# Performance work log

Hardware: AMD Instinct MI355X
Metric: run time of the kernel (lower is better)

Reference implementation:

```python
import jax, jax.numpy as jnp
import numpy as np

B, S, H = 32, 512, 768
NH, HD = 8, 96
NC = 3
SEP = 102
NEG = -1e9


def telu(x):
    return x * jnp.tanh(jnp.exp(x))


def setup_inputs() -> dict:
    rng = np.random.default_rng(0)
    key = jax.random.key(0)
    ks = jax.random.split(key, 16)
    # ragged premise/hypothesis spans: [CLS] premise [SEP] hypothesis [SEP] pad
    s1 = rng.integers(64, 256, size=B)
    s2 = rng.integers(s1 + 32, 500)
    ids = rng.integers(1000, 30000, size=(B, S))  # avoid accidental SEP ids
    for i in range(B):
        ids[i, 0] = 101
        ids[i, s1[i]] = SEP
        ids[i, s2[i]] = SEP
        ids[i, s2[i] + 1:] = 0
    pos = np.arange(S)[None, :]
    am = (pos <= s2[:, None]).astype(np.int32)

    def lin(k, i, o):
        return jax.random.normal(k, (i, o), jnp.float32) * 0.02

    return dict(
        hidden_states=jax.random.normal(ks[0], (B, S, H), jnp.float32),
        input_ids=jnp.asarray(ids, jnp.int32),
        attention_mask=jnp.asarray(am, jnp.int32),
        fe_w1=lin(ks[1], H, 512), fe_b1=jnp.zeros(512), fe_g=jnp.ones(512), fe_be=jnp.zeros(512),
        fe_w2=lin(ks[2], 512, 128), fe_b2=jnp.zeros(128),
        al_w1=lin(ks[3], 2 * H, 768), al_b1=jnp.zeros(768),
        al_w2=lin(ks[4], 768, 128), al_b2=jnp.zeros(128),
        mha_wq=lin(ks[5], H, H), mha_bq=jnp.zeros(H),
        mha_wk=lin(ks[6], H, H), mha_bk=jnp.zeros(H),
        mha_wv=lin(ks[7], H, H), mha_bv=jnp.zeros(H),
        mha_wo=lin(ks[8], H, H), mha_bo=jnp.zeros(H),
        dp_w=lin(ks[9], H, 128), dp_b=jnp.zeros(128),
        ap_w=lin(ks[10], H, 128), ap_b=jnp.zeros(128),
        cl_w1=lin(ks[11], 512, 64), cl_b1=jnp.zeros(64),
        cl_w2=lin(ks[12], 64, NC), cl_b2=jnp.zeros(NC),
    )


def reference(hidden_states, input_ids, attention_mask,
              fe_w1, fe_b1, fe_g, fe_be, fe_w2, fe_b2,
              al_w1, al_b1, al_w2, al_b2,
              mha_wq, mha_bq, mha_wk, mha_bk, mha_wv, mha_bv, mha_wo, mha_bo,
              dp_w, dp_b, ap_w, ap_b, cl_w1, cl_b1, cl_w2, cl_b2):
    hs = hidden_states
    am = attention_mask.astype(hs.dtype)
    sep = (input_ids == SEP)
    pos = jnp.arange(S)[None, :]
    s1 = jnp.argmax(sep, axis=1)            # first SEP
    s2 = (S - 1) - jnp.argmax(sep[:, ::-1], axis=1)  # second SEP
    prem = ((pos >= 1) & (pos < s1[:, None])).astype(hs.dtype)   # premise span [1, s1)
    hyp = ((pos > s1[:, None]) & (pos < s2[:, None])).astype(hs.dtype)  # hypothesis (s1, s2)

    def mmean(x, m):  # masked mean over seq: x [B,S,H], m [B,S]
        return jnp.einsum('bsh,bs->bh', x, m) / jnp.clip(m.sum(1, keepdims=True), 1e-9, None)

    # pooled + mean + max representations -> feature_extractor
    pooled = hs[:, 0]
    mean_rep = mmean(hs, am)
    max_rep = jnp.max(jnp.where(am[..., None] > 0, hs, NEG), axis=1)
    h = (pooled + mean_rep + max_rep) @ fe_w1 + fe_b1
    h = (h - h.mean(-1, keepdims=True)) / jnp.sqrt(h.var(-1, keepdims=True) + 1e-5) * fe_g + fe_be
    feat = telu(h @ fe_w2 + fe_b2)

    # sentence diff head
    sent_diff = jnp.abs(mmean(hs, prem) - mmean(hs, hyp))
    diff_rep = telu(sent_diff @ dp_w + dp_b)

    # cross attention: hypothesis queries attend to premise keys/values
    q = (hs @ mha_wq + mha_bq).reshape(B, S, NH, HD)
    k = (hs @ mha_wk + mha_bk).reshape(B, S, NH, HD)
    v = (hs @ mha_wv + mha_bv).reshape(B, S, NH, HD)
    scores = jnp.einsum('bqhd,bkhd->bhqk', q, k) / np.sqrt(HD).astype(np.float32)
    scores = jnp.where(prem[:, None, None, :] > 0, scores, NEG)
    attn = jax.nn.softmax(scores, axis=-1)
    ctx = jnp.einsum('bhqk,bkhd->bqhd', attn, v).reshape(B, S, H) @ mha_wo + mha_bo
    attn_rep = telu(mmean(ctx, hyp) @ ap_w + ap_b)

    # word alignment (both directions share one similarity matrix)
    sim = jnp.einsum('bsd,btd->bst', hs, hs)
    w_p2h = jax.nn.softmax(jnp.where(hyp[:, None, :] > 0, sim, NEG), axis=-1)
    al1 = mmean(jnp.einsum('bst,btd->bsd', w_p2h, hs), prem)
    w_h2p = jax.nn.softmax(jnp.where(prem[:, None, :] > 0, sim, NEG), axis=-1)
    al2 = mmean(jnp.einsum('bst,btd->bsd', w_h2p, hs), hyp)
    align_rep = telu((jnp.concatenate([al1, al2], -1) @ al_w1 + al_b1) @ al_w2 + al_b2)

    combined = jnp.concatenate([feat, diff_rep, attn_rep, align_rep], -1)  # [B, 512]
    logits = telu(combined @ cl_w1 + cl_b1) @ cl_w2 + cl_b2
    return logits
```

## Files before the change

kernel.cpp:

```cpp
#include <hip/hip_runtime.h>
#include <hip/hip_bf16.h>
#include <math.h>

#define SS 512
#define HH 768
#define NEGV -1e9f
#define APAD 100

typedef float f32x4 __attribute__((ext_vector_type(4)));
typedef __bf16 bf16x8 __attribute__((ext_vector_type(8)));

__device__ __forceinline__ float telu_f(float x){ return x * tanhf(expf(x)); }

__device__ __forceinline__ short f2bf(float x){
  __hip_bfloat16 h = __float2bfloat16(x);
  return __builtin_bit_cast(short, h);
}
__device__ __forceinline__ float b2f(short s){
  __hip_bfloat16 h = __builtin_bit_cast(__hip_bfloat16, s);
  return __bfloat162float(h);
}

__device__ __forceinline__ void gl_lds16(const void* g, void* l){
  __builtin_amdgcn_global_load_lds((const __attribute__((address_space(1))) void*)g,
                                   (__attribute__((address_space(3))) void*)l, 16, 0, 0);
}

__device__ __forceinline__ float wred_max(float v){
  #pragma unroll
  for (int o=32;o>0;o>>=1) v = fmaxf(v, __shfl_xor(v, o));
  return v;
}
__device__ __forceinline__ float wred_sum(float v){
  #pragma unroll
  for (int o=32;o>0;o>>=1) v += __shfl_xor(v, o);
  return v;
}

__global__ __launch_bounds__(512) void k_scan(const int* __restrict__ ids, const int* __restrict__ am,
                       int* s1a, int* s2a, float* invnam, float* invnp, float* invnh,
                       float* __restrict__ uacc, float* __restrict__ v1g, float* __restrict__ v2g){
  int b = blockIdx.x, tid = threadIdx.x;
  __shared__ int mn, mx, cnt;
  if (tid==0){ mn = 1<<30; mx = -1; cnt = 0; }
  __syncthreads();
  int id = ids[b*SS+tid];
  if (id==102){ atomicMin(&mn, tid); atomicMax(&mx, tid); }
  atomicAdd(&cnt, am[b*SS+tid]);
  #pragma unroll
  for (int i=0;i<4;i++) uacc[(size_t)b*2048 + tid + i*512] = 0.f;
  v1g[b*SS+tid] = 0.f;
  v2g[b*SS+tid] = 0.f;
  __syncthreads();
  if (tid==0){
    int s1 = mn; if (s1 > 255) s1 = 255; if (s1 < 1) s1 = 1;
    int s2 = mx; if (s2 < s1+1) s2 = s1+1; if (s2 > 511) s2 = 511;
    s1a[b]=s1; s2a[b]=s2;
    invnam[b] = 1.f/fmaxf((float)cnt, 1e-9f);
    invnp[b]  = 1.f/fmaxf((float)(s1-1), 1e-9f);
    invnh[b]  = 1.f/fmaxf((float)(s2-s1-1), 1e-9f);
  }
}

__global__ __launch_bounds__(256) void k_g2(const float* __restrict__ hs, const int* __restrict__ amask,
    const int* __restrict__ s1a, const int* __restrict__ s2a,
    short* __restrict__ hsb, short* __restrict__ hsl, float4* __restrict__ repp,
    const float* __restrict__ wq, const float* __restrict__ wk, const float* __restrict__ wv,
    short* __restrict__ Wt){
  __shared__ __align__(16) char smem[16896];
  int id = blockIdx.x, tid = threadIdx.x;
  if (id < 768){
    int b = id&31, hc = (id>>5)%6, sc = id/192;
    int* ams = (int*)smem;
    float4* rb4 = (float4*)(smem + 512);
    int sbase = sc*128;
    if (tid < 128) ams[tid] = amask[b*SS + sbase + tid];
    __syncthreads();
    int s1 = s1a[b], s2 = s2a[b];
    int hlane = tid & 31, srow = tid >> 5;
    int h0 = hc*128 + hlane*4;
    float sm[4]={0,0,0,0}, sp[4]={0,0,0,0}, sh[4]={0,0,0,0};
    float mxv[4]={NEGV,NEGV,NEGV,NEGV};
    for (int si = srow; si < 128; si += 8){
      int s = sbase + si;
      float4 x = *(const float4*)(hs + ((size_t)(b*SS+s))*HH + h0);
      float xv[4] = {x.x,x.y,x.z,x.w};
      bool am = ams[si] > 0;
      bool ip = (s>=1 && s<s1), ih = (s>s1 && s<s2);
      short hi4[4], lo4[4];
      #pragma unroll
      for (int c=0;c<4;c++){
        if (am){ sm[c]+=xv[c]; mxv[c]=fmaxf(mxv[c],xv[c]); }
        if (ip) sp[c]+=xv[c];
        if (ih) sh[c]+=xv[c];
        hi4[c] = f2bf(xv[c]);
        lo4[c] = f2bf(xv[c] - b2f(hi4[c]));
      }
      *(short4*)(hsb + ((size_t)(b*SS+s))*HH + h0) = *(short4*)hi4;
      *(short4*)(hsl + ((size_t)(b*SS+s))*HH + h0) = *(short4*)lo4;
    }
    #pragma unroll
    for (int c=0;c<4;c++) rb4[srow*128 + hlane*4+c] = make_float4(sm[c], mxv[c], sp[c], sh[c]);
    __syncthreads();
    if (tid < 128){
      float4 a = rb4[tid];
      #pragma unroll
      for (int r=1;r<8;r++){
        float4 v = rb4[r*128 + tid];
        a.x += v.x; a.y = fmaxf(a.y, v.y); a.z += v.z; a.w += v.w;
      }
      repp[(((size_t)(b*6+hc))*4 + sc)*128 + tid] = a;
    }
  } else {
    int w = id - 768;
    int k0 = (w%24)*32, n0 = ((w/24)%24)*32, which = w/576;
    const float* W = which==0? wq : (which==1? wk : wv);
    float (*tl)[33] = (float(*)[33])smem;
    int r = tid>>3, c4 = (tid&7)*4;
    float4 v = *(const float4*)(W + (size_t)(k0+r)*HH + n0 + c4);
    tl[r][c4+0]=v.x; tl[r][c4+1]=v.y; tl[r][c4+2]=v.z; tl[r][c4+3]=v.w;
    __syncthreads();
    short4 o;
    o.x = f2bf(tl[c4+0][r]); o.y = f2bf(tl[c4+1][r]);
    o.z = f2bf(tl[c4+2][r]); o.w = f2bf(tl[c4+3][r]);
    *(short4*)(Wt + (size_t)which*HH*HH + (size_t)(n0+r)*HH + k0 + c4) = o;
  }
}

__device__ __forceinline__ void build_vec(const float4* __restrict__ repp, const float* __restrict__ hs,
    const float* __restrict__ invnam, const float* __restrict__ invnp, const float* __restrict__ invnh,
    int b, int tid, bool want_sdiff, float* xs){
  for (int h = tid; h < HH; h += 256){
    int hc = h>>7, hr = h&127;
    float S=0.f, M=NEGV, P=0.f, Hh=0.f;
    #pragma unroll
    for (int sc=0; sc<4; sc++){
      float4 v = repp[(((size_t)(b*6+hc))*4 + sc)*128 + hr];
      S += v.x; M = fmaxf(M, v.y); P += v.z; Hh += v.w;
    }
    if (want_sdiff) xs[h] = fabsf(P*invnp[b] - Hh*invnh[b]);
    else            xs[h] = hs[((size_t)(b*SS))*HH + h] + S*invnam[b] + M;
  }
}

__global__ __launch_bounds__(256) void k_smallA(const float4* __restrict__ repp, const float* __restrict__ hs,
    const float* __restrict__ invnam, const float* __restrict__ invnp, const float* __restrict__ invnh,
    const float* __restrict__ fe_w1, const float* __restrict__ fe_b1, float* __restrict__ featd,
    const float* __restrict__ dpw, const float* __restrict__ dpb, float* __restrict__ comb){
  __shared__ float xs[HH];
  __shared__ float psum[2][128];
  int id = blockIdx.x, tid = threadIdx.x;
  int jj = tid & 127, half = tid >> 7;
  if (id < 128){
    int b = id&31, j0 = (id>>5)*128;
    build_vec(repp, hs, invnam, invnp, invnh, b, tid, false, xs);
    __syncthreads();
    float a = 0.f;
    #pragma unroll 8
    for (int i = half*384; i < half*384+384; i++)
      a += xs[i]*fe_w1[(size_t)i*512 + j0 + jj];
    psum[half][jj] = a;
    __syncthreads();
    if (tid < 128)
      featd[(size_t)b*512 + j0 + tid] = fe_b1[j0+tid] + psum[0][tid] + psum[1][tid];
  } else {
    int b = id - 128;
    build_vec(repp, hs, invnam, invnp, invnh, b, tid, true, xs);
    __syncthreads();
    float a = 0.f;
    #pragma unroll 8
    for (int i = half*384; i < half*384+384; i++)
      a += xs[i]*dpw[(size_t)i*128 + jj];
    psum[half][jj] = a;
    __syncthreads();
    if (tid < 128)
      comb[b*512 + 128 + tid] = telu_f(dpb[tid] + psum[0][tid] + psum[1][tid]);
  }
}

__global__ __launch_bounds__(256) void k_mm(const short* __restrict__ hsb, const short* __restrict__ hsl,
    const short* __restrict__ Wt,
    const float* __restrict__ bq, const float* __restrict__ bk, const float* __restrict__ bv,
    short* __restrict__ qbh, short* __restrict__ kbh, float* __restrict__ vb,
    const int* __restrict__ s1a, const int* __restrict__ s2a, float* __restrict__ sim){
  __shared__ __align__(16) char smem[32768];
  int id = blockIdx.x;
  int tid = threadIdx.x, lane = tid&63, wave = tid>>6;
  int wm = wave>>1, wn = wave&1;
  int lm = lane&15, lq = lane>>4;
  if (id < 1536){
    int which, local;
    if (id < 768){ which=0; local=id; }
    else if (id < 1152){ which=1; local=id-768; }
    else { which=2; local=id-1152; }
    int r8 = local & 7, n = (local>>3)%6, gq = local/48;
    int rt = gq*8 + r8;
    int n0 = n*128;
    int r0, b;
    if (which==0){ r0 = rt*128; b = r0>>9; }
    else { b = rt>>1; r0 = b*512 + (rt&1)*128; }
    int s1 = s1a[b], s2 = s2a[b];
    int s0 = r0 & (SS-1);
    if (which==0){ if (s0 >= s2 || s0 + 127 <= s1) return; }
    else { if (s0 >= s1) return; }
    const float* bias = which==0? bq : (which==1? bk : bv);
    const short* Wb = Wt + (size_t)which*HH*HH;
    short* As = (short*)smem;
    short* Bs = As + 4096;
    f32x4 acc[4][4];
    #pragma unroll
    for (int i=0;i<4;i++)
      #pragma unroll
      for (int j=0;j<4;j++) acc[i][j] = (f32x4){0.f,0.f,0.f,0.f};
    for (int k0=0;k0<HH;k0+=32){
      __syncthreads();
      #pragma unroll
      for (int t=0;t<2;t++){
        int c = tid + t*256;
        int ib = c>>6, l = c&63;
        int row = ib*16 + (l&15);
        int kk  = k0 + (l>>4)*8;
        gl_lds16(hsb + (size_t)(r0+row)*HH + kk, As + c*8);
        gl_lds16(Wb  + (size_t)(n0+row)*HH + kk, Bs + c*8);
      }
      __syncthreads();
      bf16x8 af[4], bfv[4];
      #pragma unroll
      for (int i=0;i<4;i++) af[i]  = *(const bf16x8*)&As[((wm*4+i)*64 + lane)*8];
      #pragma unroll
      for (int j=0;j<4;j++) bfv[j] = *(const bf16x8*)&Bs[((wn*4+j)*64 + lane)*8];
      #pragma unroll
      for (int i=0;i<4;i++)
        #pragma unroll
        for (int j=0;j<4;j++)
          acc[i][j] = __builtin_amdgcn_mfma_f32_16x16x32_bf16(af[i], bfv[j], acc[i][j], 0, 0, 0);
    }
    #pragma unroll
    for (int i=0;i<4;i++){
      #pragma unroll
      for (int j=0;j<4;j++){
        int col = n0 + wn*64 + j*16 + lm;
        float bcol = bias[col];
        #pragma unroll
        for (int r4=0;r4<4;r4++){
          int row = r0 + wm*64 + i*16 + lq*4 + r4;
          int s = row & (SS-1);
          float val = acc[i][j][r4] + bcol;
          if (which==0){
            if (s > s1 && s < s2) qbh[(size_t)row*HH + col] = f2bf(val);
          } else if (s >= 1 && s < s1){
            size_t o = ((size_t)(b*256+s))*HH + col;
            if (which==1) kbh[o] = f2bf(val); else vb[o] = val;
          }
        }
      }
    }
  } else {
    int local = id - 1536;
    int b = (local&7) + 8*(local>>7);
    int t = (local>>3)&15;
    int s0 = (t>>2)*128, t0 = (t&3)*128;
    int s2 = s2a[b];
    if (s0 >= s2 || t0 >= s2) return;
    short* Ah = (short*)smem;
    short* Al = Ah + 4096;
    short* Bh = Ah + 8192;
    short* Bl = Ah + 12288;
    const size_t base = (size_t)b*SS*HH;
    f32x4 acc[4][4];
    #pragma unroll
    for (int i=0;i<4;i++)
      #pragma unroll
      for (int j=0;j<4;j++) acc[i][j] = (f32x4){0.f,0.f,0.f,0.f};
    for (int k0=0;k0<HH;k0+=32){
      __syncthreads();
      #pragma unroll
      for (int t2=0;t2<2;t2++){
        int c = tid + t2*256;
        int ib = c>>6, l = c&63;
        int row = ib*16 + (l&15);
        int kk  = k0 + (l>>4)*8;
        gl_lds16(hsb + base + (size_t)(s0+row)*HH + kk, Ah + c*8);
        gl_lds16(hsl + base + (size_t)(s0+row)*HH + kk, Al + c*8);
        gl_lds16(hsb + base + (size_t)(t0+row)*HH + kk, Bh + c*8);
        gl_lds16(hsl + base + (size_t)(t0+row)*HH + kk, Bl + c*8);
      }
      __syncthreads();
      bf16x8 ah[4], al[4], bh[4], bl[4];
      #pragma unroll
      for (int i=0;i<4;i++){
        ah[i] = *(const bf16x8*)&Ah[((wm*4+i)*64 + lane)*8];
        al[i] = *(const bf16x8*)&Al[((wm*4+i)*64 + lane)*8];
      }
      #pragma unroll
      for (int j=0;j<4;j++){
        bh[j] = *(const bf16x8*)&Bh[((wn*4+j)*64 + lane)*8];
        bl[j] = *(const bf16x8*)&Bl[((wn*4+j)*64 + lane)*8];
      }
      #pragma unroll
      for (int i=0;i<4;i++)
        #pragma unroll
        for (int j=0;j<4;j++){
          acc[i][j] = __builtin_amdgcn_mfma_f32_16x16x32_bf16(ah[i], bh[j], acc[i][j], 0, 0, 0);
          acc[i][j] = __builtin_amdgcn_mfma_f32_16x16x32_bf16(ah[i], bl[j], acc[i][j], 0, 0, 0);
          acc[i][j] = __builtin_amdgcn_mfma_f32_16x16x32_bf16(al[i], bh[j], acc[i][j], 0, 0, 0);
        }
    }
    #pragma unroll
    for (int i=0;i<4;i++){
      #pragma unroll
      for (int j=0;j<4;j++){
        int col = t0 + wn*64 + j*16 + lm;
        #pragma unroll
        for (int r4=0;r4<4;r4++){
          int row = s0 + wm*64 + i*16 + lq*4 + r4;
          sim[((size_t)(b*SS+row))*SS + col] = acc[i][j][r4];
        }
      }
    }
  }
}

__global__ __launch_bounds__(256) void k_attn_simsm(const short* __restrict__ qbh, const short* __restrict__ kbh,
    const int* __restrict__ s1a, const int* __restrict__ s2a, float* __restrict__ uacc,
    const float* __restrict__ sim, float* __restrict__ v1g, float* __restrict__ v2g){
  __shared__ __align__(16) char smem[64000];
  int id = blockIdx.x, tid = threadIdx.x;
  int wave = tid>>6, lane = tid&63;
  if (id < 2048){
    int b = id&31, h = (id>>5)&7, zc = id>>8;
    int s1 = s1a[b], s2 = s2a[b];
    int qs = s1 + 1 + zc*64;
    if (qs >= s2) return;
    short* Ks = (short*)smem;
    short* Qs = Ks + 256*APAD;
    int lm = lane&15, lq = lane>>4;
    int jmax = (s1+15)>>4;
    int krows = jmax<<4;
    for (int i = tid; i < krows*12; i += 256){
      int r = i/12, c = i - r*12;
      *(int4*)&Ks[r*APAD + c*8] = *(const int4*)(kbh + ((size_t)(b*256+r))*HH + h*96 + c*8);
    }
    for (int i = tid; i < 64*12; i += 256){
      int r = i/12, c = i - r*12;
      int q = qs + r;
      int4 v = {0,0,0,0};
      if (q < SS) v = *(const int4*)(qbh + ((size_t)(b*SS+q))*HH + h*96 + c*8);
      *(int4*)&Qs[r*APAD + c*8] = v;
    }
    __syncthreads();
    f32x4 acc[16];
    #pragma unroll
    for (int j=0;j<16;j++) acc[j] = (f32x4){0.f,0.f,0.f,0.f};
    #pragma unroll
    for (int ks=0; ks<3; ks++){
      bf16x8 a = *(const bf16x8*)&Qs[(wave*16+lm)*APAD + ks*32 + lq*8];
      #pragma unroll
      for (int j=0;j<16;j++){
        if (j < jmax){
          bf16x8 bfr = *(const bf16x8*)&Ks[(j*16+lm)*APAD + ks*32 + lq*8];
          acc[j] = __builtin_amdgcn_mfma_f32_16x16x32_bf16(a, bfr, acc[j], 0, 0, 0);
        }
      }
    }
    const float scale = 0.1020620726f;
    float uj[16];
    #pragma unroll
    for (int j=0;j<16;j++) uj[j]=0.f;
    int qrow_base = qs + wave*16 + lq*4;
    #pragma unroll
    for (int r=0;r<4;r++){
      float m = -1e30f;
      float sc[16];
      #pragma unroll
      for (int j=0;j<16;j++){
        int c = j*16 + lm;
        float s = (c>=1 && c<s1) ? acc[j][r]*scale : -1e30f;
        sc[j] = s; m = fmaxf(m, s);
      }
      #pragma unroll
      for (int o=1;o<16;o<<=1) m = fmaxf(m, __shfl_xor(m, o));
      float ssum = 0.f;
      #pragma unroll
      for (int j=0;j<16;j++){ float p = expf(sc[j]-m); sc[j]=p; ssum += p; }
      #pragma unroll
      for (int o=1;o<16;o<<=1) ssum += __shfl_xor(ssum, o);
      bool rvalid = (qrow_base + r) < s2;
      float inv = rvalid ? 1.f/ssum : 0.f;
      #pragma unroll
      for (int j=0;j<16;j++) uj[j] += sc[j]*inv;
    }
    #pragma unroll
    for (int j=0;j<16;j++){
      if (j < jmax){
        float v = uj[j];
        v += __shfl_xor(v, 16);
        v += __shfl_xor(v, 32);
        if (lq==0 && v != 0.f)
          atomicAdd(&uacc[((size_t)(b*8+h))*256 + j*16 + lm], v);
      }
    }
  } else {
    int l = id - 2048;
    int b = l&31, cy = l>>5;
    int s1 = s1a[b], s2 = s2a[b];
    int r0 = cy*64;
    float* av = (float*)smem;
    for (int i=tid;i<2*4*SS;i+=256) av[i]=0.f;
    __syncthreads();
    for (int r = r0 + wave; r < r0+64; r += 4){
      int t0,t1,which;
      if (r>=1 && r<s1){ t0=s1+1; t1=s2; which=0; }
      else if (r>s1 && r<s2){ t0=1; t1=s1; which=1; }
      else continue;
      const float* row = sim + ((size_t)(b*SS+r))*SS;
      float vals[7]; float mx=-1e30f;
      #pragma unroll
      for (int j=0;j<7;j++){
        int t = t0 + lane + 64*j;
        vals[j] = (t<t1) ? row[t] : -1e30f;
        mx = fmaxf(mx, vals[j]);
      }
      mx = wred_max(mx);
      float ssum=0.f;
      #pragma unroll
      for (int j=0;j<7;j++){
        int t = t0+lane+64*j;
        vals[j] = (t<t1)? expf(vals[j]-mx) : 0.f;
        ssum += vals[j];
      }
      ssum = wred_sum(ssum);
      float inv = 1.f/ssum;
      #pragma unroll
      for (int j=0;j<7;j++){
        int t = t0+lane+64*j;
        if (t<t1) av[(which*4 + wave)*SS + t] += vals[j]*inv;
      }
    }
    __syncthreads();
    for (int t=tid;t<SS;t+=256){
      float a0 = av[0*SS+t]+av[1*SS+t]+av[2*SS+t]+av[3*SS+t];
      float a1 = av[4*SS+t]+av[5*SS+t]+av[6*SS+t]+av[7*SS+t];
      if (a0 != 0.f) atomicAdd(&v1g[b*SS+t], a0);
      if (a1 != 0.f) atomicAdd(&v2g[b*SS+t], a1);
    }
  }
}

__global__ __launch_bounds__(256) void k_ctx_alvec(const float* __restrict__ uacc, const float* __restrict__ vb,
    const int* __restrict__ s1a, const float* __restrict__ invnh, float* __restrict__ cmg,
    const float* __restrict__ hs, const float* __restrict__ v1g, const float* __restrict__ v2g,
    const float* __restrict__ invnp, float* __restrict__ catg){
  __shared__ __align__(16) char smem[9216];
  int id = blockIdx.x, tid = threadIdx.x;
  if (id < 192){
    int b = id&31, i0 = (id>>5)*128;
    int s1 = s1a[b]; int nk = s1-1;
    float inh = invnh[b];
    float* us = (float*)smem;
    float* ps = us + 2048;
    for (int idx=tid; idx<2048; idx+=256) us[idx] = uacc[(size_t)b*2048 + idx];
    __syncthreads();
    int ii = tid & 127, half = tid >> 7;
    int i = i0 + ii;
    int h = i/96;
    float a = 0.f;
    int lo = 1 + half*128;
    int hi = nk < (lo+127) ? nk : (lo+127);
    for (int sl=lo; sl<=hi; sl++)
      a += us[h*256+sl]*vb[((size_t)(b*256+sl))*HH + i];
    ps[half*128 + ii] = a;
    __syncthreads();
    if (tid < 128)
      cmg[(size_t)b*HH + i0 + tid] = (ps[tid] + ps[128+tid])*inh;
  } else {
    int l = id - 192;
    int b = l&31, d0 = (l>>5)*64;
    float* sv1 = (float*)smem;
    float* sv2 = sv1 + 512;
    float* p1  = sv2 + 512;
    float* p2  = p1 + 256;
    for (int t=tid;t<SS;t+=256){ sv1[t]=v1g[b*SS+t]; sv2[t]=v2g[b*SS+t]; }
    __syncthreads();
    int d = d0 + (tid&63), ch = tid>>6;
    float a1=0.f, a2=0.f;
    for (int t=ch*128; t<ch*128+128; t++){
      float x = hs[((size_t)(b*SS+t))*HH + d];
      a1 += sv1[t]*x; a2 += sv2[t]*x;
    }
    p1[ch*64 + (tid&63)]=a1; p2[ch*64 + (tid&63)]=a2;
    __syncthreads();
    if (tid < 64){
      float s1_ = p1[tid]+p1[64+tid]+p1[128+tid]+p1[192+tid];
      float s2_ = p2[tid]+p2[64+tid]+p2[128+tid]+p2[192+tid];
      catg[(size_t)b*1536 + d0 + tid]       = s1_*invnp[b];
      catg[(size_t)b*1536 + 768 + d0 + tid] = s2_*invnh[b];
    }
  }
}

template<int K>
__device__ __forceinline__ void gemv_ct(const float* __restrict__ x, const float* __restrict__ W,
    const float* __restrict__ bias, float* __restrict__ y, int b, int j0, int tid,
    float* xs, float* psum){
  for (int i=tid;i<K;i+=256) xs[i] = x[(size_t)b*K + i];
  __syncthreads();
  int jj = tid & 127, half = tid >> 7;
  int j = j0 + jj;
  float a = 0.f;
  #pragma unroll 8
  for (int i = half*(K/2); i < (half+1)*(K/2); i++)
    a += xs[i]*W[(size_t)i*HH + j];
  psum[half*128 + jj] = a;
  __syncthreads();
  if (tid < 128)
    y[(size_t)b*HH + j0 + tid] = bias[j0+tid] + psum[tid] + psum[128+tid];
}

__global__ __launch_bounds__(256) void k_gemvB(const float* __restrict__ cmg, const float* __restrict__ wo,
    const float* __restrict__ bo, float* __restrict__ accg,
    const float* __restrict__ catg, const float* __restrict__ al_w1, const float* __restrict__ al_b1,
    float* __restrict__ tmpg){
  __shared__ float xs[1536];
  __shared__ float psum[256];
  int id = blockIdx.x, tid = threadIdx.x;
  if (id < 192){
    gemv_ct<768>(cmg, wo, bo, accg, id&31, (id>>5)*128, tid, xs, psum);
  } else {
    int l = id-192;
    gemv_ct<1536>(catg, al_w1, al_b1, tmpg, l&31, (l>>5)*128, tid, xs, psum);
  }
}

__global__ __launch_bounds__(256) void k_tailsC(const float* __restrict__ accg, const float* __restrict__ apw,
    const float* __restrict__ apb, const float* __restrict__ tmpg, const float* __restrict__ al_w2,
    const float* __restrict__ al_b2, float* __restrict__ comb,
    const float* __restrict__ featd, const float* __restrict__ g, const float* __restrict__ be,
    const float* __restrict__ w2, const float* __restrict__ b2){
  __shared__ __align__(16) float smem[1664];
  int id = blockIdx.x, tid = threadIdx.x;
  if (id < 64){
    float* xs = smem;
    float* psum = smem + HH;
    const float *x, *W, *bias; int b, off;
    if (id < 32){ b = id; x=accg; W=apw; bias=apb; off=256; }
    else { b = id-32; x=tmpg; W=al_w2; bias=al_b2; off=384; }
    for (int i=tid;i<HH;i+=256) xs[i] = x[(size_t)b*HH + i];
    __syncthreads();
    int jj = tid & 127, half = tid >> 7;
    float a = 0.f;
    #pragma unroll 8
    for (int i = half*384; i < half*384+384; i++)
      a += xs[i]*W[(size_t)i*128 + jj];
    psum[half*128 + jj] = a;
    __syncthreads();
    if (tid < 128)
      comb[b*512 + off + tid] = telu_f(bias[tid] + psum[tid] + psum[128+tid]);
  } else {
    int b = id - 64;
    float* hv  = smem;
    float* hn  = hv + 512;
    float* red = hn + 512;
    float* ps  = red + 256;
    hv[tid] = featd[(size_t)b*512 + tid];
    hv[tid+256] = featd[(size_t)b*512 + tid + 256];
    __syncthreads();
    red[tid] = hv[tid] + hv[tid+256];
    __syncthreads();
    for (int st=128; st>0; st>>=1){ if (tid<st) red[tid]+=red[tid+st]; __syncthreads(); }
    float mean = red[0]*(1.f/512.f);
    __syncthreads();
    float d0 = hv[tid]-mean, d1 = hv[tid+256]-mean;
    red[tid] = d0*d0 + d1*d1;
    __syncthreads();
    for (int st=128; st>0; st>>=1){ if (tid<st) red[tid]+=red[tid+st]; __syncthreads(); }
    float inv = 1.f/sqrtf(red[0]*(1.f/512.f) + 1e-5f);
    __syncthreads();
    hn[tid]     = d0*inv*g[tid]     + be[tid];
    hn[tid+256] = d1*inv*g[tid+256] + be[tid+256];
    __syncthreads();
    int jj = tid & 127, half = tid >> 7;
    float a = 0.f;
    #pragma unroll 8
    for (int k = half*256; k < half*256+256; k++)
      a += hn[k]*w2[k*128 + jj];
    ps[half*128 + jj] = a;
    __syncthreads();
    if (tid < 128)
      comb[b*512 + tid] = telu_f(b2[tid] + ps[tid] + ps[128+tid]);
  }
}

__global__ __launch_bounds__(64) void k_cls(const float* __restrict__ comb,
    const float* __restrict__ w1, const float* __restrict__ b1,
    const float* __restrict__ w2, const float* __restrict__ b2, float* __restrict__ out){
  int b=blockIdx.x, tid=threadIdx.x;
  __shared__ float cb[512];
  __shared__ float t1[64];
  for (int i=tid;i<512;i+=64) cb[i]=comb[b*512+i];
  __syncthreads();
  float a = b1[tid];
  for (int k=0;k<512;k++) a += cb[k]*w1[(size_t)k*64+tid];
  t1[tid]=telu_f(a);
  __syncthreads();
  if (tid<3){
    float o = b2[tid];
    for (int k=0;k<64;k++) o += t1[k]*w2[k*3+tid];
    out[b*3+tid]=o;
  }
}

extern "C" void kernel_launch(void* const* d_in, const int* in_sizes, int n_in,
                              void* d_out, int out_size, void* d_ws, size_t ws_size,
                              hipStream_t stream){
  const float* hs   = (const float*)d_in[0];
  const int*   ids  = (const int*)d_in[1];
  const int*   amask= (const int*)d_in[2];
  const float* fe_w1= (const float*)d_in[3];
  const float* fe_b1= (const float*)d_in[4];
  const float* fe_g = (const float*)d_in[5];
  const float* fe_be= (const float*)d_in[6];
  const float* fe_w2= (const float*)d_in[7];
  const float* fe_b2= (const float*)d_in[8];
  const float* al_w1= (const float*)d_in[9];
  const float* al_b1= (const float*)d_in[10];
  const float* al_w2= (const float*)d_in[11];
  const float* al_b2= (const float*)d_in[12];
  const float* wq   = (const float*)d_in[13];
  const float* bq   = (const float*)d_in[14];
  const float* wk   = (const float*)d_in[15];
  const float* bk   = (const float*)d_in[16];
  const float* wv   = (const float*)d_in[17];
  const float* bv   = (const float*)d_in[18];
  const float* wo   = (const float*)d_in[19];
  const float* bo   = (const float*)d_in[20];
  const float* dpw  = (const float*)d_in[21];
  const float* dpb  = (const float*)d_in[22];
  const float* apw  = (const float*)d_in[23];
  const float* apb  = (const float*)d_in[24];
  const float* clw1 = (const float*)d_in[25];
  const float* clb1 = (const float*)d_in[26];
  const float* clw2 = (const float*)d_in[27];
  const float* clb2 = (const float*)d_in[28];
  float* out = (float*)d_out;

  char* base = (char*)d_ws;
  size_t off = 0;
  auto alloc = [&](size_t bytes)->char*{ char* p = base + off; off += (bytes + 255) & ~(size_t)255; return p; };
  short* hsb  = (short*)alloc((size_t)32*SS*HH*2);
  short* hsl  = (short*)alloc((size_t)32*SS*HH*2);
  short* Wt   = (short*)alloc((size_t)3*HH*HH*2);
  short* qbh  = (short*)alloc((size_t)32*SS*HH*2);
  short* kbh  = (short*)alloc((size_t)32*256*HH*2);
  float* vb   = (float*)alloc((size_t)32*256*HH*4);
  float* simb = (float*)alloc((size_t)32*SS*SS*4);
  float* uacc = (float*)alloc((size_t)32*8*256*4);
  float* v1g  = (float*)alloc((size_t)32*SS*4);
  float* v2g  = (float*)alloc((size_t)32*SS*4);
  int*   s1a  = (int*)alloc(32*4);
  int*   s2a  = (int*)alloc(32*4);
  float* invnam=(float*)alloc(32*4);
  float* invnp =(float*)alloc(32*4);
  float* invnh =(float*)alloc(32*4);
  float* comb = (float*)alloc((size_t)32*512*4);
  float4* repp= (float4*)alloc((size_t)32*6*4*128*16);
  float* featd= (float*)alloc((size_t)32*512*4);
  float* catg = (float*)alloc((size_t)32*1536*4);
  float* tmpg = (float*)alloc((size_t)32*HH*4);
  float* cmg  = (float*)alloc((size_t)32*HH*4);
  float* accg = (float*)alloc((size_t)32*HH*4);

  k_scan<<<dim3(32), dim3(512), 0, stream>>>(ids, amask, s1a, s2a, invnam, invnp, invnh, uacc, v1g, v2g);
  k_g2<<<dim3(2496), dim3(256), 0, stream>>>(hs, amask, s1a, s2a, hsb, hsl, repp, wq, wk, wv, Wt);
  k_mm<<<dim3(2048), dim3(256), 0, stream>>>(hsb, hsl, Wt, bq, bk, bv, qbh, kbh, vb, s1a, s2a, simb);
  k_smallA<<<dim3(160), dim3(256), 0, stream>>>(repp, hs, invnam, invnp, invnh, fe_w1, fe_b1, featd, dpw, dpb, comb);
  k_attn_simsm<<<dim3(2304), dim3(256), 0, stream>>>(qbh, kbh, s1a, s2a, uacc, simb, v1g, v2g);
  k_ctx_alvec<<<dim3(576), dim3(256), 0, stream>>>(uacc, vb, s1a, invnh, cmg, hs, v1g, v2g, invnp, catg);
  k_gemvB<<<dim3(384), dim3(256), 0, stream>>>(cmg, wo, bo, accg, catg, al_w1, al_b1, tmpg);
  k_tailsC<<<dim3(96), dim3(256), 0, stream>>>(accg, apw, apb, tmpg, al_w2, al_b2, comb,
                                               featd, fe_g, fe_be, fe_w2, fe_b2);
  k_cls<<<dim3(32), dim3(64), 0, stream>>>(comb, clw1, clb1, clw2, clb2, out);
}
```

Measured before the change: 544.4 us.

## Double-buffer LDS in k_mm GEMMs, reorder sim blocks first, fold k_smallA in

The QKV projection and similarity GEMM tiles now double-buffer their LDS staging, so the global-to-LDS loads for the next k-slice are issued while MFMAs run on the current one. The heavier similarity blocks are moved to the start of the grid so they are scheduled early. The small gemv kernel k_smallA is merged into k_mm as extra trailing blocks, removing one launch and letting that work overlap with the GEMM tail. LDS per block grows to 64KB, which may reduce occupancy.

```diff
diff --git a/kernel.cpp b/kernel.cpp
--- a/kernel.cpp
+++ b/kernel.cpp
@@ -143,56 +143,99 @@
   }
 }
 
-__global__ __launch_bounds__(256) void k_smallA(const float4* __restrict__ repp, const float* __restrict__ hs,
-    const float* __restrict__ invnam, const float* __restrict__ invnp, const float* __restrict__ invnh,
-    const float* __restrict__ fe_w1, const float* __restrict__ fe_b1, float* __restrict__ featd,
-    const float* __restrict__ dpw, const float* __restrict__ dpb, float* __restrict__ comb){
-  __shared__ float xs[HH];
-  __shared__ float psum[2][128];
-  int id = blockIdx.x, tid = threadIdx.x;
-  int jj = tid & 127, half = tid >> 7;
-  if (id < 128){
-    int b = id&31, j0 = (id>>5)*128;
-    build_vec(repp, hs, invnam, invnp, invnh, b, tid, false, xs);
-    __syncthreads();
-    float a = 0.f;
-    #pragma unroll 8
-    for (int i = half*384; i < half*384+384; i++)
-      a += xs[i]*fe_w1[(size_t)i*512 + j0 + jj];
-    psum[half][jj] = a;
-    __syncthreads();
-    if (tid < 128)
-      featd[(size_t)b*512 + j0 + tid] = fe_b1[j0+tid] + psum[0][tid] + psum[1][tid];
-  } else {
-    int b = id - 128;
-    build_vec(repp, hs, invnam, invnp, invnh, b, tid, true, xs);
-    __syncthreads();
-    float a = 0.f;
-    #pragma unroll 8
-    for (int i = half*384; i < half*384+384; i++)
-      a += xs[i]*dpw[(size_t)i*128 + jj];
-    psum[half][jj] = a;
-    __syncthreads();
-    if (tid < 128)
-      comb[b*512 + 128 + tid] = telu_f(dpb[tid] + psum[0][tid] + psum[1][tid]);
-  }
-}
-
 __global__ __launch_bounds__(256) void k_mm(const short* __restrict__ hsb, const short* __restrict__ hsl,
     const short* __restrict__ Wt,
     const float* __restrict__ bq, const float* __restrict__ bk, const float* __restrict__ bv,
     short* __restrict__ qbh, short* __restrict__ kbh, float* __restrict__ vb,
-    const int* __restrict__ s1a, const int* __restrict__ s2a, float* __restrict__ sim){
-  __shared__ __align__(16) char smem[32768];
+    const int* __restrict__ s1a, const int* __restrict__ s2a, float* __restrict__ sim,
+    const float4* __restrict__ repp, const float* __restrict__ hs,
+    const float* __restrict__ invnam, const float* __restrict__ invnp, const float* __restrict__ invnh,
+    const float* __restrict__ fe_w1, const float* __restrict__ fe_b1, float* __restrict__ featd,
+    const float* __restrict__ dpw, const float* __restrict__ dpb, float* __restrict__ comb){
+  __shared__ __align__(16) short smem_s[32768];
   int id = blockIdx.x;
   int tid = threadIdx.x, lane = tid&63, wave = tid>>6;
   int wm = wave>>1, wn = wave&1;
   int lm = lane&15, lq = lane>>4;
-  if (id < 1536){
+  if (id < 512){
+    int local = id;
+    int b = (local&7) + 8*(local>>7);
+    int t = (local>>3)&15;
+    int s0 = (t>>2)*128, t0 = (t&3)*128;
+    int s2 = s2a[b];
+    if (s0 >= s2 || t0 >= s2) return;
+    const size_t base = (size_t)b*SS*HH;
+    auto stage = [&](int k0, int bufi){
+      short* Ah = smem_s + bufi*16384;
+      short* Al = Ah + 4096;
+      short* Bh = Ah + 8192;
+      short* Bl = Ah + 12288;
+      #pragma unroll
+      for (int t2=0;t2<2;t2++){
+        int c = tid + t2*256;
+        int ib = c>>6, l = c&63;
+        int row = ib*16 + (l&15);
+        int kk  = k0 + (l>>4)*8;
+        gl_lds16(hsb + base + (size_t)(s0+row)*HH + kk, Ah + c*8);
+        gl_lds16(hsl + base + (size_t)(s0+row)*HH + kk, Al + c*8);
+        gl_lds16(hsb + base + (size_t)(t0+row)*HH + kk, Bh + c*8);
+        gl_lds16(hsl + base + (size_t)(t0+row)*HH + kk, Bl + c*8);
+      }
+    };
+    f32x4 acc[4][4];
+    #pragma unroll
+    for (int i=0;i<4;i++)
+      #pragma unroll
+      for (int j=0;j<4;j++) acc[i][j] = (f32x4){0.f,0.f,0.f,0.f};
+    stage(0, 0);
+    __syncthreads();
+    int bufi = 0;
+    for (int k0=0;k0<HH;k0+=32){
+      if (k0+32 < HH) stage(k0+32, bufi^1);
+      short* Ah = smem_s + bufi*16384;
+      short* Al = Ah + 4096;
+      short* Bh = Ah + 8192;
+      short* Bl = Ah + 12288;
+      bf16x8 ah[4], al[4], bh[4], bl[4];
+      #pragma unroll
+      for (int i=0;i<4;i++){
+        ah[i] = *(const bf16x8*)&Ah[((wm*4+i)*64 + lane)*8];
+        al[i] = *(const bf16x8*)&Al[((wm*4+i)*64 + lane)*8];
+      }
+      #pragma unroll
+      for (int j=0;j<4;j++){
+        bh[j] = *(const bf16x8*)&Bh[((wn*4+j)*64 + lane)*8];
+        bl[j] = *(const bf16x8*)&Bl[((wn*4+j)*64 + lane)*8];
+      }
+      #pragma unroll
+      for (int i=0;i<4;i++)
+        #pragma unroll
+        for (int j=0;j<4;j++){
+          acc[i][j] = __builtin_amdgcn_mfma_f32_16x16x32_bf16(ah[i], bh[j], acc[i][j], 0, 0, 0);
+          acc[i][j] = __builtin_amdgcn_mfma_f32_16x16x32_bf16(ah[i], bl[j], acc[i][j], 0, 0, 0);
+          acc[i][j] = __builtin_amdgcn_mfma_f32_16x16x32_bf16(al[i], bh[j], acc[i][j], 0, 0, 0);
+        }
+      __syncthreads();
+      bufi ^= 1;
+    }
+    #pragma unroll
+    for (int i=0;i<4;i++){
+      #pragma unroll
+      for (int j=0;j<4;j++){
+        int col = t0 + wn*64 + j*16 + lm;
+        #pragma unroll
+        for (int r4=0;r4<4;r4++){
+          int row = s0 + wm*64 + i*16 + lq*4 + r4;
+          sim[((size_t)(b*SS+row))*SS + col] = acc[i][j][r4];
+        }
+      }
+    }
+  } else if (id < 2048){
     int which, local;
-    if (id < 768){ which=0; local=id; }
-    else if (id < 1152){ which=1; local=id-768; }
-    else { which=2; local=id-1152; }
+    int qid = id - 512;
+    if (qid < 768){ which=0; local=qid; }
+    else if (qid < 1152){ which=1; local=qid-768; }
+    else { which=2; local=qid-1152; }
     int r8 = local & 7, n = (local>>3)%6, gq = local/48;
     int rt = gq*8 + r8;
     int n0 = n*128;
@@ -205,25 +248,31 @@
     else { if (s0 >= s1) return; }
     const float* bias = which==0? bq : (which==1? bk : bv);
     const short* Wb = Wt + (size_t)which*HH*HH;
-    short* As = (short*)smem;
-    short* Bs = As + 4096;
-    f32x4 acc[4][4];
-    #pragma unroll
-    for (int i=0;i<4;i++)
-      #pragma unroll
-      for (int j=0;j<4;j++) acc[i][j] = (f32x4){0.f,0.f,0.f,0.f};
-    for (int k0=0;k0<HH;k0+=32){
-      __syncthreads();
-      #pragma unroll
-      for (int t=0;t<2;t++){
-        int c = tid + t*256;
+    auto stageq = [&](int k0, int bufi){
+      short* As = smem_s + bufi*8192;
+      short* Bs = As + 4096;
+      #pragma unroll
+      for (int t2=0;t2<2;t2++){
+        int c = tid + t2*256;
         int ib = c>>6, l = c&63;
         int row = ib*16 + (l&15);
         int kk  = k0 + (l>>4)*8;
         gl_lds16(hsb + (size_t)(r0+row)*HH + kk, As + c*8);
         gl_lds16(Wb  + (size_t)(n0+row)*HH + kk, Bs + c*8);
       }
-      __syncthreads();
+    };
+    f32x4 acc[4][4];
+    #pragma unroll
+    for (int i=0;i<4;i++)
+      #pragma unroll
+      for (int j=0;j<4;j++) acc[i][j] = (f32x4){0.f,0.f,0.f,0.f};
+    stageq(0, 0);
+    __syncthreads();
+    int bufi = 0;
+    for (int k0=0;k0<HH;k0+=32){
+      if (k0+32 < HH) stageq(k0+32, bufi^1);
+      short* As = smem_s + bufi*8192;
+      short* Bs = As + 4096;
       bf16x8 af[4], bfv[4];
       #pragma unroll
       for (int i=0;i<4;i++) af[i]  = *(const bf16x8*)&As[((wm*4+i)*64 + lane)*8];
@@ -234,6 +283,8 @@
         #pragma unroll
         for (int j=0;j<4;j++)
           acc[i][j] = __builtin_amdgcn_mfma_f32_16x16x32_bf16(af[i], bfv[j], acc[i][j], 0, 0, 0);
+      __syncthreads();
+      bufi ^= 1;
     }
     #pragma unroll
     for (int i=0;i<4;i++){
@@ -256,67 +307,34 @@
       }
     }
   } else {
-    int local = id - 1536;
-    int b = (local&7) + 8*(local>>7);
-    int t = (local>>3)&15;
-    int s0 = (t>>2)*128, t0 = (t&3)*128;
-    int s2 = s2a[b];
-    if (s0 >= s2 || t0 >= s2) return;
-    short* Ah = (short*)smem;
-    short* Al = Ah + 4096;
-    short* Bh = Ah + 8192;
-    short* Bl = Ah + 12288;
-    const size_t base = (size_t)b*SS*HH;
-    f32x4 acc[4][4];
-    #pragma unroll
-    for (int i=0;i<4;i++)
-      #pragma unroll
-      for (int j=0;j<4;j++) acc[i][j] = (f32x4){0.f,0.f,0.f,0.f};
-    for (int k0=0;k0<HH;k0+=32){
+    int sid = id - 2048;
+    float* xs = (float*)smem_s;
+    float* psum = xs + HH;
+    int jj = tid & 127, half = tid >> 7;
+    if (sid < 128){
+      int b = sid&31, j0 = (sid>>5)*128;
+      build_vec(repp, hs, invnam, invnp, invnh, b, tid, false, xs);
       __syncthreads();
-      #pragma unroll
-      for (int t2=0;t2<2;t2++){
-        int c = tid + t2*256;
-        int ib = c>>6, l = c&63;
-        int row = ib*16 + (l&15);
-        int kk  = k0 + (l>>4)*8;
-        gl_lds16(hsb + base + (size_t)(s0+row)*HH + kk, Ah + c*8);
-        gl_lds16(hsl + base + (size_t)(s0+row)*HH + kk, Al + c*8);
-        gl_lds16(hsb + base + (size_t)(t0+row)*HH + kk, Bh + c*8);
-        gl_lds16(hsl + base + (size_t)(t0+row)*HH + kk, Bl + c*8);
-      }
+      float a = 0.f;
+      #pragma unroll 8
+      for (int i = half*384; i < half*384+384; i++)
+        a += xs[i]*fe_w1[(size_t)i*512 + j0 + jj];
+      psum[half*128 + jj] = a;
       __syncthreads();
-      bf16x8 ah[4], al[4], bh[4], bl[4];
-      #pragma unroll
-      for (int i=0;i<4;i++){
-        ah[i] = *(const bf16x8*)&Ah[((wm*4+i)*64 + lane)*8];
-        al[i] = *(const bf16x8*)&Al[((wm*4+i)*64 + lane)*8];
-      }
-      #pragma unroll
-      for (int j=0;j<4;j++){
-        bh[j] = *(const bf16x8*)&Bh[((wn*4+j)*64 + lane)*8];
-        bl[j] = *(const bf16x8*)&Bl[((wn*4+j)*64 + lane)*8];
-      }
-      #pragma unroll
-      for (int i=0;i<4;i++)
-        #pragma unroll
-        for (int j=0;j<4;j++){
-          acc[i][j] = __builtin_amdgcn_mfma_f32_16x16x32_bf16(ah[i], bh[j], acc[i][j], 0, 0, 0);
-          acc[i][j] = __builtin_amdgcn_mfma_f32_16x16x32_bf16(ah[i], bl[j], acc[i][j], 0, 0, 0);
-          acc[i][j] = __builtin_amdgcn_mfma_f32_16x16x32_bf16(al[i], bh[j], acc[i][j], 0, 0, 0);
-        }
-    }
-    #pragma unroll
-    for (int i=0;i<4;i++){
-      #pragma unroll
-      for (int j=0;j<4;j++){
-        int col = t0 + wn*64 + j*16 + lm;
-        #pragma unroll
-        for (int r4=0;r4<4;r4++){
-          int row = s0 + wm*64 + i*16 + lq*4 + r4;
-          sim[((size_t)(b*SS+row))*SS + col] = acc[i][j][r4];
-        }
-      }
+      if (tid < 128)
+        featd[(size_t)b*512 + j0 + tid] = fe_b1[j0+tid] + psum[tid] + psum[128+tid];
+    } else {
+      int b = sid - 128;
+      build_vec(repp, hs, invnam, invnp, invnh, b, tid, true, xs);
+      __syncthreads();
+      float a = 0.f;
+      #pragma unroll 8
+      for (int i = half*384; i < half*384+384; i++)
+        a += xs[i]*dpw[(size_t)i*128 + jj];
+      psum[half*128 + jj] = a;
+      __syncthreads();
+      if (tid < 128)
+        comb[b*512 + 128 + tid] = telu_f(dpb[tid] + psum[tid] + psum[128+tid]);
     }
   }
 }
@@ -672,8 +690,8 @@
 
   k_scan<<<dim3(32), dim3(512), 0, stream>>>(ids, amask, s1a, s2a, invnam, invnp, invnh, uacc, v1g, v2g);
   k_g2<<<dim3(2496), dim3(256), 0, stream>>>(hs, amask, s1a, s2a, hsb, hsl, repp, wq, wk, wv, Wt);
-  k_mm<<<dim3(2048), dim3(256), 0, stream>>>(hsb, hsl, Wt, bq, bk, bv, qbh, kbh, vb, s1a, s2a, simb);
-  k_smallA<<<dim3(160), dim3(256), 0, stream>>>(repp, hs, invnam, invnp, invnh, fe_w1, fe_b1, featd, dpw, dpb, comb);
+  k_mm<<<dim3(2208), dim3(256), 0, stream>>>(hsb, hsl, Wt, bq, bk, bv, qbh, kbh, vb, s1a, s2a, simb,
+                                             repp, hs, invnam, invnp, invnh, fe_w1, fe_b1, featd, dpw, dpb, comb);
   k_attn_simsm<<<dim3(2304), dim3(256), 0, stream>>>(qbh, kbh, s1a, s2a, uacc, simb, v1g, v2g);
   k_ctx_alvec<<<dim3(576), dim3(256), 0, stream>>>(uacc, vb, s1a, invnh, cmg, hs, v1g, v2g, invnp, catg);
   k_gemvB<<<dim3(384), dim3(256), 0, stream>>>(cmg, wo, bo, accg, catg, al_w1, al_b1, tmpg);
```

New measurement: 510.4 us. 6.2% less time.
